# Performance work log

Measured on AMD Instinct MI355X. Metric: run time of the kernel, lower is better.

## Reference

```python
import jax, jax.numpy as jnp
import numpy as np

B, C, H, W = 8, 256, 128, 128
HEADS, WS = 8, 8
SHIFT = WS // 2  # type=='W' -> shift_size = window_size//2 in this repo
N = WS * WS


def _rel_pos_index(ws):
    coords = np.stack(np.meshgrid(np.arange(ws), np.arange(ws), indexing='ij')).reshape(2, -1)
    rel = (coords[:, :, None] - coords[:, None, :]).transpose(1, 2, 0)  # N,N,2
    rel[:, :, 0] += ws - 1
    rel[:, :, 1] += ws - 1
    rel[:, :, 0] *= 2 * ws - 1
    return rel.sum(-1)  # (N,N) ints in [0,(2ws-1)^2)


def _attn_mask(h, w, ws, shift):
    img = np.zeros((h, w), np.int32)
    cnt = 0
    for hs in (slice(0, -ws), slice(-ws, -shift), slice(-shift, None)):
        for wsl in (slice(0, -ws), slice(-ws, -shift), slice(-shift, None)):
            img[hs, wsl] = cnt
            cnt += 1
    m = img.reshape(h // ws, ws, w // ws, ws).transpose(0, 2, 1, 3).reshape(-1, ws * ws)
    diff = m[:, None, :] - m[:, :, None]
    return np.where(diff != 0, -100.0, 0.0).astype(np.float32)  # (nW,N,N)


def _ln(x, w, b, eps=1e-5):
    mu = jnp.mean(x, -1, keepdims=True)
    var = jnp.mean(jnp.square(x - mu), -1, keepdims=True)
    return (x - mu) * jax.lax.rsqrt(var + eps) * w + b


def setup_inputs() -> dict:
    key = jax.random.key(0)
    ks = jax.random.split(key, 10)
    s = 0.02
    return {
        'x': jax.random.normal(ks[0], (B, C, H, W), jnp.float32),
        'ln1_w': jnp.ones((C,), jnp.float32),
        'ln1_b': jnp.zeros((C,), jnp.float32),
        'qkv_w': jax.random.normal(ks[1], (3 * C, C), jnp.float32) * s,
        'qkv_b': jnp.zeros((3 * C,), jnp.float32),
        'rel_bias': jax.random.normal(ks[2], ((2 * WS - 1) ** 2, HEADS), jnp.float32) * s,
        'proj_w': jax.random.normal(ks[3], (C, C), jnp.float32) * s,
        'proj_b': jnp.zeros((C,), jnp.float32),
        'ln2_w': jnp.ones((C,), jnp.float32),
        'ln2_b': jnp.zeros((C,), jnp.float32),
        'fc1_w': jax.random.normal(ks[4], (4 * C, C), jnp.float32) * s,
        'fc1_b': jnp.zeros((4 * C,), jnp.float32),
        'fc2_w': jax.random.normal(ks[5], (C, 4 * C), jnp.float32) * s,
        'fc2_b': jnp.zeros((C,), jnp.float32),
    }


def reference(x, ln1_w, ln1_b, qkv_w, qkv_b, rel_bias, proj_w, proj_b,
              ln2_w, ln2_b, fc1_w, fc1_b, fc2_w, fc2_b):
    b, c, h, w = x.shape
    hd = c // HEADS
    scale = hd ** -0.5
    nW = (h // WS) * (w // WS)

    t = x.transpose(0, 2, 3, 1).reshape(b, h * w, c)  # b (hw) c
    shortcut = t
    t = _ln(t, ln1_w, ln1_b).reshape(b, h, w, c)
    t = jnp.roll(t, (-SHIFT, -SHIFT), axis=(1, 2))  # cyclic shift
    # window partition -> (b*nW, N, c)
    win = t.reshape(b, h // WS, WS, w // WS, WS, c).transpose(0, 1, 3, 2, 4, 5).reshape(b * nW, N, c)

    qkv = (win @ qkv_w.T + qkv_b).reshape(b * nW, N, 3, HEADS, hd).transpose(2, 0, 3, 1, 4)
    q, k, v = qkv[0], qkv[1], qkv[2]  # (b*nW, heads, N, hd)
    attn = jnp.einsum('bhnd,bhmd->bhnm', q * scale, k)
    rpi = jnp.asarray(_rel_pos_index(WS))
    bias = rel_bias[rpi.reshape(-1)].reshape(N, N, HEADS).transpose(2, 0, 1)  # (heads,N,N)
    attn = attn + bias[None]
    mask = jnp.asarray(_attn_mask(h, w, WS, SHIFT))  # (nW,N,N)
    attn = attn.reshape(b, nW, HEADS, N, N) + mask[None, :, None]
    attn = jax.nn.softmax(attn, axis=-1).reshape(b * nW, HEADS, N, N)
    out = jnp.einsum('bhnm,bhmd->bhnd', attn, v).transpose(0, 2, 1, 3).reshape(b * nW, N, c)
    out = out @ proj_w.T + proj_b
    # window reverse + reverse shift
    out = out.reshape(b, h // WS, w // WS, WS, WS, c).transpose(0, 1, 3, 2, 4, 5).reshape(b, h, w, c)
    out = jnp.roll(out, (SHIFT, SHIFT), axis=(1, 2)).reshape(b, h * w, c)

    t = shortcut + out
    h2 = _ln(t, ln2_w, ln2_b)
    h2 = jax.nn.gelu(h2 @ fc1_w.T + fc1_b)
    t = t + (h2 @ fc2_w.T + fc2_b)
    return t.reshape(b, h, w, c).transpose(0, 3, 1, 2)
```

## Files before the change

### kernel.cpp

```cpp
#include <hip/hip_runtime.h>
#include <cstdint>
#include <cstddef>

using f32x4 = __attribute__((ext_vector_type(4))) float;
using bf16x8 = __attribute__((ext_vector_type(8))) __bf16;
using u16x4 = __attribute__((ext_vector_type(4))) unsigned short;
using u16x8 = __attribute__((ext_vector_type(8))) unsigned short;

#define DEV __device__ __forceinline__

DEV unsigned short f2b(float f) {
  __bf16 h = (__bf16)f;
  return __builtin_bit_cast(unsigned short, h);
}
DEV float b2f(unsigned short u) {
  uint32_t w = ((uint32_t)u) << 16;
  return __builtin_bit_cast(float, w);
}

DEV void gload16(const unsigned short* g, unsigned short* l) {
  __builtin_amdgcn_global_load_lds(
      (const __attribute__((address_space(1))) void*)g,
      (__attribute__((address_space(3))) void*)l, 16, 0, 0);
}

DEV void waitv(int n) {
  switch (n) {
    case 0: asm volatile("s_waitcnt vmcnt(0)" ::: "memory"); break;
    case 2: asm volatile("s_waitcnt vmcnt(2)" ::: "memory"); break;
    case 3: asm volatile("s_waitcnt vmcnt(3)" ::: "memory"); break;
    case 8: asm volatile("s_waitcnt vmcnt(8)" ::: "memory"); break;
    default: asm volatile("s_waitcnt vmcnt(0)" ::: "memory"); break;
  }
}


__global__ void swin_cvt_all(const float* __restrict__ qkvw, const float* __restrict__ projw,
                             const float* __restrict__ fc1w, const float* __restrict__ fc2w,
                             unsigned short* __restrict__ wq, unsigned short* __restrict__ wp,
                             unsigned short* __restrict__ w1, unsigned short* __restrict__ w2) {
  int i = blockIdx.x * 256 + threadIdx.x;
  if (i < 196608) wq[i] = f2b(qkvw[i]);
  else if (i < 262144) wp[i - 196608] = f2b(projw[i - 196608]);
  else if (i < 524288) w1[i - 262144] = f2b(fc1w[i - 262144]);
  else w2[i - 524288] = f2b(fc2w[i - 524288]);
}

__global__ void swin_btab(const float* __restrict__ relb, float* __restrict__ bt) {
  int id = blockIdx.x * 256 + threadIdx.x;
  int m = id & 63, n = (id >> 6) & 63, head = (id >> 12) & 7, cls = id >> 15;
  bool eh = cls & 2, ew = cls & 1;
  int nh = n >> 3, nw = n & 7, mh = m >> 3, mw = m & 7;
  int rn = (eh ? ((nh >> 2) + 1) : 0) * 3 + (ew ? ((nw >> 2) + 1) : 0);
  int rm = (eh ? ((mh >> 2) + 1) : 0) * 3 + (ew ? ((mw >> 2) + 1) : 0);
  float v = relb[(size_t)((nh - mh + 7) * 15 + (nw - mw + 7)) * 8 + head];
  if (rn != rm) v -= 100.f;
  bt[id] = v;
}

__global__ __launch_bounds__(256)
void swin_ln1win(const float* __restrict__ x,
                 const float* __restrict__ lw, const float* __restrict__ lb,
                 unsigned short* __restrict__ win, unsigned short* __restrict__ xb) {
  __shared__ float sh[512];
  __shared__ float mean_[128], rstd_[128];
  __shared__ unsigned short tile[128 * 136];
  int bh = blockIdx.x; int b = bh >> 7, h = bh & 127;
  int t = threadIdx.x;
  int w = t & 127, ch = t >> 7;
  const float* px = x + (((size_t)(b * 256 + ch * 128)) << 14) + (h << 7) + w;
  float s = 0.f, s2 = 0.f;
  for (int c = 0; c < 128; ++c) {
    float v = px[(size_t)c << 14];
    s += v; s2 += v * v;
  }
  sh[t] = s; sh[256 + t] = s2;
  __syncthreads();
  if (ch == 0) {
    s += sh[t + 128]; s2 += sh[256 + t + 128];
    float mu = s * (1.f / 256.f);
    mean_[w] = mu;
    rstd_[w] = rsqrtf(s2 * (1.f / 256.f) - mu * mu + 1e-5f);
  }
  int hp = (h + 124) & 127;
  int whh = hp >> 3, nh = hp & 7;
  int lg = t & 31, grp = t >> 5;
#pragma unroll
  for (int half = 0; half < 2; ++half) {
    int c0 = half << 7;
    __syncthreads();
#pragma unroll
    for (int i = 0; i < 64; ++i) {
      int cr = (i << 1) + ch;
      float v = x[(((size_t)(b * 256 + c0 + cr)) << 14) + (h << 7) + w];
      tile[w * 136 + cr] = f2b(v);
    }
    __syncthreads();
#pragma unroll
    for (int i = 0; i < 16; ++i) {
      int w2 = (i << 3) + grp;
      u16x4 raw = *(const u16x4*)&tile[w2 * 136 + (lg << 2)];
      float mu = mean_[w2], rs = rstd_[w2];
      int c = c0 + (lg << 2);
      f32x4 lwv = *(const f32x4*)(lw + c);
      f32x4 lbv = *(const f32x4*)(lb + c);
      u16x4 o;
#pragma unroll
      for (int k = 0; k < 4; ++k)
        o[k] = f2b((b2f(raw[k]) - mu) * rs * lwv[k] + lbv[k]);
      int wp_ = (w2 + 124) & 127;
      int wwc = wp_ >> 3, nw = wp_ & 7;
      size_t wt = (size_t)b * 256 + whh * 16 + wwc;
      int n = (nh << 3) + nw;
      *(u16x4*)&win[((wt << 6) + n) * 256 + c] = o;
      *(u16x4*)&xb[(((size_t)bh << 7) + w2) * 256 + c] = raw;
    }
  }
}

template<int MODE, int KTOT>
__global__ __launch_bounds__(512, 2)
void swin_gemm(const unsigned short* __restrict__ A,
               const unsigned short* __restrict__ Wt,
               const float* __restrict__ bias,
               void* __restrict__ outp,
               const void* __restrict__ extra,
               int M, int N,
               const float* __restrict__ lw2 = nullptr,
               const float* __restrict__ lb2 = nullptr,
               unsigned short* __restrict__ tn = nullptr) {
  constexpr int KT = KTOT / 64;
  __shared__ __align__(16) unsigned short As[2][16384];
  __shared__ __align__(16) unsigned short Bs[2][16384];
  const int cpx = gridDim.x >> 3;
  const int bid = (blockIdx.x & 7) * cpx + (blockIdx.x >> 3);
  const int nbn = N >> 8;
  const int bm = bid / nbn;
  const int bn = bid % nbn;
  const int m0 = bm << 8, n0 = bn << 8;
  const int t = threadIdx.x;
  const int lane = t & 63;
  const int wave = t >> 6;
  const int wr = wave >> 2, wc = wave & 3;
  const int cl = lane & 15, g = lane >> 4;

  const int trow = t >> 3;
  const int ks = (t & 7) ^ (trow & 7);
  const unsigned short* agb = A  + (size_t)(m0 + trow) * KTOT + ks * 8;
  const unsigned short* bgb = Wt + (size_t)(n0 + trow) * KTOT + ks * 8;

  const int ra = wr * 128 + cl;
  const int rb = wc * 64 + cl;
  const int ka0 = (g ^ (cl & 7)) * 8;

  auto stage = [&](int buf, int kt) {
    const int ko = kt * 64;
#pragma unroll
    for (int l = 0; l < 4; ++l) {
      gload16(agb + (size_t)l * 64 * KTOT + ko, &As[buf][l * 4096 + t * 8]);
      gload16(bgb + (size_t)l * 64 * KTOT + ko, &Bs[buf][l * 4096 + t * 8]);
    }
  };

  f32x4 acc[8][4] = {};
  bf16x8 afA[8], bfA[4], afB[8], bfB[4];

  auto RD = [&](int buf, int kk, bf16x8* af, bf16x8* bfr) {
    const int ka = ka0 ^ (kk << 5);
#pragma unroll
    for (int i = 0; i < 8; ++i)
      af[i] = *(const bf16x8*)&As[buf][(ra + i * 16) * 64 + ka];
#pragma unroll
    for (int j = 0; j < 4; ++j)
      bfr[j] = *(const bf16x8*)&Bs[buf][(rb + j * 16) * 64 + ka];
  };
  auto MF = [&](bf16x8* af, bf16x8* bfr) {
    __builtin_amdgcn_s_setprio(1);
#pragma unroll
    for (int i = 0; i < 8; ++i)
#pragma unroll
      for (int j = 0; j < 4; ++j)
        acc[i][j] = __builtin_amdgcn_mfma_f32_16x16x32_bf16(bfr[j], af[i], acc[i][j], 0, 0, 0);
    __builtin_amdgcn_s_setprio(0);
  };

  stage(0, 0);
  stage(1, 1);
  waitv(8);
  __builtin_amdgcn_s_barrier();
  RD(0, 0, afA, bfA);
#pragma unroll
  for (int kt = 0; kt < KT; ++kt) {
    const int cur = kt & 1;
    RD(cur, 1, afB, bfB);
    MF(afA, bfA);
    asm volatile("s_waitcnt lgkmcnt(0)" ::: "memory");
    __builtin_amdgcn_sched_barrier(0);
    __builtin_amdgcn_s_barrier();
    if (kt + 2 < KT) stage(cur, kt + 2);
    if (kt + 1 < KT) waitv(8);
    else             waitv(0);
    __builtin_amdgcn_s_barrier();
    if (kt + 1 < KT) RD(cur ^ 1, 0, afA, bfA);
    MF(afB, bfB);
  }

  if constexpr (MODE == 1) {
    float s[8], s2v[8];
#pragma unroll
    for (int i = 0; i < 8; ++i) { s[i] = 0.f; s2v[i] = 0.f; }
#pragma unroll
    for (int i = 0; i < 8; ++i) {
      int row = m0 + wr * 128 + i * 16 + cl;
#pragma unroll
      for (int j = 0; j < 4; ++j) {
        int colb = wc * 64 + j * 16 + (g << 2);
        f32x4 b4 = *(const f32x4*)(bias + colb);
        u16x4 xv = *(const u16x4*)((const unsigned short*)extra + (size_t)row * 256 + colb);
#pragma unroll
        for (int r = 0; r < 4; ++r) {
          float v = acc[i][j][r] + b4[r] + b2f(xv[r]);
          acc[i][j][r] = v;
          s[i] += v; s2v[i] += v * v;
        }
      }
    }
#pragma unroll
    for (int i = 0; i < 8; ++i) {
      s[i]  += __shfl_xor(s[i], 16);  s[i]  += __shfl_xor(s[i], 32);
      s2v[i] += __shfl_xor(s2v[i], 16); s2v[i] += __shfl_xor(s2v[i], 32);
    }
    __syncthreads();
    float* lsum = (float*)&As[0][0];
    if (g == 0) {
#pragma unroll
      for (int i = 0; i < 8; ++i) {
        int rl = wr * 128 + i * 16 + cl;
        lsum[wc * 256 + rl] = s[i];
        lsum[1024 + wc * 256 + rl] = s2v[i];
      }
    }
    __syncthreads();
#pragma unroll
    for (int i = 0; i < 8; ++i) {
      int rl = wr * 128 + i * 16 + cl;
      float ts = lsum[rl] + lsum[256 + rl] + lsum[512 + rl] + lsum[768 + rl];
      float ts2 = lsum[1024 + rl] + lsum[1280 + rl] + lsum[1536 + rl] + lsum[1792 + rl];
      float mu = ts * (1.f / 256.f);
      float rstd = rsqrtf(ts2 * (1.f / 256.f) - mu * mu + 1e-5f);
      int row = m0 + rl;
#pragma unroll
      for (int j = 0; j < 4; ++j) {
        int colb = wc * 64 + j * 16 + (g << 2);
        f32x4 wv = *(const f32x4*)(lw2 + colb);
        f32x4 bv = *(const f32x4*)(lb2 + colb);
        u16x4 oT, on;
#pragma unroll
        for (int r = 0; r < 4; ++r) {
          float v = acc[i][j][r];
          oT[r] = f2b(v);
          on[r] = f2b((v - mu) * rstd * wv[r] + bv[r]);
        }
        *(u16x4*)((unsigned short*)outp + (size_t)row * 256 + colb) = oT;
        *(u16x4*)(tn + (size_t)row * 256 + colb) = on;
      }
    }
  } else {
#pragma unroll
    for (int i = 0; i < 8; ++i) {
      int row = m0 + wr * 128 + i * 16 + cl;
#pragma unroll
      for (int j = 0; j < 4; ++j) {
        int colb = n0 + wc * 64 + j * 16 + (g << 2);
        f32x4 b4 = *(const f32x4*)(bias + colb);
        const bool qs = (n0 == 0);
        u16x4 o;
#pragma unroll
        for (int r = 0; r < 4; ++r) {
          float v = acc[i][j][r] + b4[r];
          if (qs) v *= 0.17677669529663687f;
          o[r] = f2b(v);
        }
        *(u16x4*)((unsigned short*)outp + (size_t)row * 768 + colb) = o;
      }
    }
  }
}

__global__ __launch_bounds__(512, 2)
void swin_ffn(const unsigned short* __restrict__ tn,
              const unsigned short* __restrict__ w1,
              const unsigned short* __restrict__ w2,
              const float* __restrict__ b1,
              const float* __restrict__ b2,
              const unsigned short* __restrict__ T,
              float* __restrict__ out) {
  __shared__ __align__(16) unsigned short As[2][4096];
  __shared__ __align__(16) unsigned short Bs[2][8192];
  __shared__ __align__(16) unsigned short Hs[32768];
  const int cpx = gridDim.x >> 3;
  const int bid = (blockIdx.x & 7) * cpx + (blockIdx.x >> 3);
  const int m0 = bid << 7;
  const int t = threadIdx.x;
  const int lane = t & 63;
  const int wave = t >> 6;
  const int wr = wave >> 2, wc = wave & 3;
  const int cl = lane & 15, g = lane >> 4;

  const int arow = t >> 2;
  const int ks = (t & 3) ^ ((arow >> 1) & 3);
  const unsigned short* ag = tn + (size_t)(m0 + arow) * 256 + ks * 8;

  const int ka = (g ^ ((cl >> 1) & 3)) * 8;
  const int ra = wr * 64 + cl;
  const int rb = wc * 64 + cl;

  auto stage1 = [&](int buf, int q, int kt) {
    gload16(ag + kt * 32, &As[buf][t * 8]);
    const unsigned short* wg = w1 + (size_t)(q * 256 + arow) * 256 + kt * 32 + ks * 8;
    gload16(wg, &Bs[buf][t * 8]);
    gload16(wg + 32768, &Bs[buf][4096 + t * 8]);
  };
  auto stage2 = [&](int buf, int q, int kt) {
    const unsigned short* wg = w2 + (size_t)arow * 1024 + q * 256 + kt * 32 + ks * 8;
    gload16(wg, &Bs[buf][t * 8]);
    gload16(wg + 131072, &Bs[buf][4096 + t * 8]);
  };

  f32x4 acc2[4][4] = {};
  bf16x8 af[4], bf[4];

  auto RD1 = [&](int buf) {
#pragma unroll
    for (int i = 0; i < 4; ++i)
      af[i] = *(const bf16x8*)&As[buf][(ra + i * 16) * 32 + ka];
#pragma unroll
    for (int j = 0; j < 4; ++j)
      bf[j] = *(const bf16x8*)&Bs[buf][(rb + j * 16) * 32 + ka];
  };
  auto RD2 = [&](int buf, int kt) {
#pragma unroll
    for (int i = 0; i < 4; ++i) {
      int row = ra + i * 16;
      int c = (kt * 4 + g) ^ (row & 7);
      af[i] = *(const bf16x8*)((const char*)Hs + row * 512 + c * 16);
    }
#pragma unroll
    for (int j = 0; j < 4; ++j)
      bf[j] = *(const bf16x8*)&Bs[buf][(rb + j * 16) * 32 + ka];
  };

  for (int q = 0; q < 4; ++q) {
    f32x4 acc1[4][4] = {};
    stage1(0, q, 0); stage1(1, q, 1);
#pragma unroll
    for (int kt = 0; kt < 8; ++kt) {
      const int cur = kt & 1;
      waitv(kt < 7 ? 3 : 0);
      __builtin_amdgcn_s_barrier();
      RD1(cur);
      asm volatile("s_waitcnt lgkmcnt(0)" ::: "memory");
      __builtin_amdgcn_sched_barrier(0);
      __builtin_amdgcn_s_barrier();
      if (kt + 2 < 8) stage1(cur, q, kt + 2);
      __builtin_amdgcn_s_setprio(1);
#pragma unroll
      for (int i = 0; i < 4; ++i)
#pragma unroll
        for (int j = 0; j < 4; ++j)
          acc1[i][j] = __builtin_amdgcn_mfma_f32_16x16x32_bf16(bf[j], af[i], acc1[i][j], 0, 0, 0);
      __builtin_amdgcn_s_setprio(0);
    }
    stage2(0, q, 0); stage2(1, q, 1);
#pragma unroll
    for (int i = 0; i < 4; ++i) {
      int row = wr * 64 + i * 16 + cl;
#pragma unroll
      for (int j = 0; j < 4; ++j) {
        int colb = wc * 64 + j * 16 + (g << 2);
        f32x4 b4 = *(const f32x4*)(b1 + q * 256 + colb);
        u16x4 o;
#pragma unroll
        for (int r = 0; r < 4; ++r) {
          float v = acc1[i][j][r] + b4[r];
          float p = v * fmaf(v * v, -0.0713548256f, -1.5957691216f);
          float e = __expf(p);
          o[r] = f2b(v * __builtin_amdgcn_rcpf(1.f + e));
        }
        int swz = (colb >> 3) ^ (row & 7);
        *(u16x4*)((char*)Hs + row * 512 + swz * 16 + ((g & 1) * 8)) = o;
      }
    }
    asm volatile("s_waitcnt lgkmcnt(0)" ::: "memory");
    __builtin_amdgcn_sched_barrier(0);
    __builtin_amdgcn_s_barrier();
#pragma unroll
    for (int kt = 0; kt < 8; ++kt) {
      const int cur = kt & 1;
      waitv(kt < 7 ? 2 : 0);
      __builtin_amdgcn_s_barrier();
      RD2(cur, kt);
      asm volatile("s_waitcnt lgkmcnt(0)" ::: "memory");
      __builtin_amdgcn_sched_barrier(0);
      __builtin_amdgcn_s_barrier();
      if (kt + 2 < 8) stage2(cur, q, kt + 2);
      __builtin_amdgcn_s_setprio(1);
#pragma unroll
      for (int i = 0; i < 4; ++i)
#pragma unroll
        for (int j = 0; j < 4; ++j)
          acc2[i][j] = __builtin_amdgcn_mfma_f32_16x16x32_bf16(bf[j], af[i], acc2[i][j], 0, 0, 0);
      __builtin_amdgcn_s_setprio(0);
    }
  }

#pragma unroll
  for (int i = 0; i < 4; ++i) {
    int row = m0 + wr * 64 + i * 16 + cl;
    int b = row >> 14, hw = row & 16383;
#pragma unroll
    for (int j = 0; j < 4; ++j) {
      int colb = wc * 64 + j * 16 + (g << 2);
      f32x4 b4 = *(const f32x4*)(b2 + colb);
      u16x4 tv = *(const u16x4*)(T + (size_t)row * 256 + colb);
#pragma unroll
      for (int r = 0; r < 4; ++r)
        out[((size_t)(b * 256 + colb + r) << 14) + hw] = acc2[i][j][r] + b4[r] + b2f(tv[r]);
    }
  }
}

__global__ __launch_bounds__(256)
void swin_attn(const unsigned short* __restrict__ qkv,
               const float* __restrict__ btab,
               unsigned short* __restrict__ attn_out) {
  __shared__ unsigned short Plds[4][64 * 68];
  __shared__ unsigned short Vlds[4][32 * 68];
  int bid = blockIdx.x;
  int w = bid >> 1, hg = bid & 1;
  int t = threadIdx.x;
  int wave = t >> 6, lane = t & 63;
  int head = (hg << 2) + wave;
  int cl = lane & 15, g = lane >> 4;
  const size_t wb = (size_t)w * 64 * 768;

  bf16x8 qf[4], kf[4];
#pragma unroll
  for (int ni = 0; ni < 4; ++ni) {
    int n = (ni << 4) + cl;
    qf[ni] = *(const bf16x8*)(qkv + wb + (size_t)n * 768 + (head << 5) + (g << 3));
    kf[ni] = *(const bf16x8*)(qkv + wb + (size_t)n * 768 + 256 + (head << 5) + (g << 3));
  }

  f32x4 s[4][4] = {};
#pragma unroll
  for (int mi = 0; mi < 4; ++mi)
#pragma unroll
    for (int ni = 0; ni < 4; ++ni)
      s[mi][ni] = __builtin_amdgcn_mfma_f32_16x16x32_bf16(kf[mi], qf[ni], s[mi][ni], 0, 0, 0);

#pragma unroll
  for (int c = 0; c < 4; ++c) {
    int id = (c << 6) + lane;
    int m = id >> 2, dc = (id & 3) << 3;
    u16x8 vv = *(const u16x8*)(qkv + wb + (size_t)m * 768 + 512 + (head << 5) + dc);
#pragma unroll
    for (int j = 0; j < 8; ++j)
      Vlds[wave][(dc + j) * 68 + m] = vv[j];
  }

  int wi = w & 255;
  int cls = (((wi >> 4) == 15) ? 2 : 0) + (((wi & 15) == 15) ? 1 : 0);
  const float* bt = btab + (((size_t)(cls << 3) + head) << 12);
#pragma unroll
  for (int ni = 0; ni < 4; ++ni) {
    int n = (ni << 4) + cl;
    float mx = -1e30f;
#pragma unroll
    for (int mi = 0; mi < 4; ++mi) {
      f32x4 bb = *(const f32x4*)&bt[n * 64 + (mi << 4) + (g << 2)];
#pragma unroll
      for (int r = 0; r < 4; ++r) {
        float v = s[mi][ni][r] + bb[r];
        s[mi][ni][r] = v;
        mx = fmaxf(mx, v);
      }
    }
    mx = fmaxf(mx, __shfl_xor(mx, 16));
    mx = fmaxf(mx, __shfl_xor(mx, 32));
    float sum = 0.f;
#pragma unroll
    for (int mi = 0; mi < 4; ++mi)
#pragma unroll
      for (int r = 0; r < 4; ++r) {
        float p = __expf(s[mi][ni][r] - mx);
        s[mi][ni][r] = p;
        sum += p;
      }
    sum += __shfl_xor(sum, 16);
    sum += __shfl_xor(sum, 32);
    float inv = __builtin_amdgcn_rcpf(sum);
#pragma unroll
    for (int mi = 0; mi < 4; ++mi) {
      u16x4 pk;
#pragma unroll
      for (int r = 0; r < 4; ++r) pk[r] = f2b(s[mi][ni][r] * inv);
      *(u16x4*)&Plds[wave][n * 68 + (mi << 4) + (g << 2)] = pk;
    }
  }
  __syncthreads();

  union FragU { bf16x8 v; uint64_t q[2]; };
  f32x4 o[4][2] = {};
#pragma unroll
  for (int mt = 0; mt < 2; ++mt) {
    FragU vf[2];
#pragma unroll
    for (int dt = 0; dt < 2; ++dt) {
      int d = (dt << 4) + cl;
      const unsigned short* p = &Vlds[wave][d * 68 + (mt << 5) + (g << 3)];
      vf[dt].q[0] = *(const uint64_t*)p;
      vf[dt].q[1] = *(const uint64_t*)(p + 4);
    }
#pragma unroll
    for (int ni = 0; ni < 4; ++ni) {
      FragU pa;
      const unsigned short* pp = &Plds[wave][((ni << 4) + cl) * 68 + (mt << 5) + (g << 3)];
      pa.q[0] = *(const uint64_t*)pp;
      pa.q[1] = *(const uint64_t*)(pp + 4);
#pragma unroll
      for (int dt = 0; dt < 2; ++dt)
        o[ni][dt] = __builtin_amdgcn_mfma_f32_16x16x32_bf16(pa.v, vf[dt].v, o[ni][dt], 0, 0, 0);
    }
  }

  int b = w >> 8;
#pragma unroll
  for (int ni = 0; ni < 4; ++ni)
#pragma unroll
    for (int dt = 0; dt < 2; ++dt)
#pragma unroll
      for (int r = 0; r < 4; ++r) {
        int n = (ni << 4) + (g << 2) + r;
        int d = (dt << 4) + cl;
        int hs = ((wi >> 4) << 3) + (n >> 3), ws_ = ((wi & 15) << 3) + (n & 7);
        int hh = (hs + 4) & 127, ww = (ws_ + 4) & 127;
        size_t tok = ((size_t)b << 14) + (hh << 7) + ww;
        attn_out[tok * 256 + (head << 5) + d] = f2b(o[ni][dt][r]);
      }
}

extern "C" void kernel_launch(void* const* d_in, const int* in_sizes, int n_in,
                              void* d_out, int out_size, void* d_ws, size_t ws_size,
                              hipStream_t stream) {
  const float* x    = (const float*)d_in[0];
  const float* ln1w = (const float*)d_in[1];
  const float* ln1b = (const float*)d_in[2];
  const float* qkvw = (const float*)d_in[3];
  const float* qkvb = (const float*)d_in[4];
  const float* relb = (const float*)d_in[5];
  const float* projw = (const float*)d_in[6];
  const float* projb = (const float*)d_in[7];
  const float* ln2w = (const float*)d_in[8];
  const float* ln2b = (const float*)d_in[9];
  const float* fc1w = (const float*)d_in[10];
  const float* fc1b = (const float*)d_in[11];
  const float* fc2w = (const float*)d_in[12];
  const float* fc2b = (const float*)d_in[13];

  char* ws = (char*)d_ws;
  unsigned short* win = (unsigned short*)(ws);
  unsigned short* qkv = (unsigned short*)(ws + 67108864);
  unsigned short* T   = (unsigned short*)(ws + 268435456);
  unsigned short* xb  = (unsigned short*)(ws + 335544320);
  unsigned short* wq  = (unsigned short*)(ws + 402653184);
  unsigned short* wp  = (unsigned short*)(ws + 403046400);
  unsigned short* w1  = (unsigned short*)(ws + 403177472);
  unsigned short* w2  = (unsigned short*)(ws + 403701760);
  float* btab         = (float*)(ws + 404226048);
  unsigned short* attn_out = win;
  unsigned short* tn  = (unsigned short*)(ws + 67108864);

  if (ws_size < 404750336ull) return;

  swin_cvt_all<<<3072, 256, 0, stream>>>(qkvw, projw, fc1w, fc2w, wq, wp, w1, w2);
  swin_btab<<<512, 256, 0, stream>>>(relb, btab);
  swin_ln1win<<<1024, 256, 0, stream>>>(x, ln1w, ln1b, win, xb);
  swin_gemm<0, 256><<<1536, 512, 0, stream>>>(win, wq, qkvb, qkv, nullptr, 131072, 768);
  swin_attn<<<4096, 256, 0, stream>>>(qkv, btab, attn_out);
  swin_gemm<1, 256><<<512, 512, 0, stream>>>(attn_out, wp, projb, T, xb, 131072, 256,
                                             ln2w, ln2b, tn);
  swin_ffn<<<1024, 512, 0, stream>>>(tn, w1, w2, fc1b, fc2b, T, (float*)d_out);
}
```

Measured before the change: 578.0 us.

## Fuse QKV projection into windowed attention kernel and retile FFN second GEMM

Replaces the separate QKV GEMM and attention kernels with a single per-window kernel. Each block loads one 64-token window into LDS, computes Q/K/V for all 8 heads with MFMA reading weights straight from global, and runs softmax attention from LDS, so the large QKV intermediate never round-trips through HBM. The proj GEMM is specialised to N=256. The FFN second GEMM now uses 64-wide K tiles with a per-quarter hidden layout, larger B staging and fewer pipeline steps. The trade-offs are that the fused kernel uses about 130KB of LDS per block, which limits occupancy, and it re-reads the QKV weights from global/L2 for every window.

New measurement: 539.8 us. -6.6%, faster.

```diff
diff --git a/kernel.cpp b/kernel.cpp
--- a/kernel.cpp
+++ b/kernel.cpp
@@ -27,8 +27,8 @@
 DEV void waitv(int n) {
   switch (n) {
     case 0: asm volatile("s_waitcnt vmcnt(0)" ::: "memory"); break;
-    case 2: asm volatile("s_waitcnt vmcnt(2)" ::: "memory"); break;
     case 3: asm volatile("s_waitcnt vmcnt(3)" ::: "memory"); break;
+    case 4: asm volatile("s_waitcnt vmcnt(4)" ::: "memory"); break;
     case 8: asm volatile("s_waitcnt vmcnt(8)" ::: "memory"); break;
     default: asm volatile("s_waitcnt vmcnt(0)" ::: "memory"); break;
   }
@@ -118,26 +118,195 @@
   }
 }
 
-template<int MODE, int KTOT>
+__global__ __launch_bounds__(512)
+void swin_qkvattn(const unsigned short* __restrict__ win,
+                  const unsigned short* __restrict__ wq,
+                  const float* __restrict__ qkvb,
+                  const float* __restrict__ btab,
+                  unsigned short* __restrict__ attn_out) {
+  __shared__ __align__(16) char L[133120];
+  const int wt = blockIdx.x;
+  const int t = threadIdx.x;
+  const int lane = t & 63;
+  const int head = t >> 6;
+  const int cl = lane & 15, g = lane >> 4;
+
+  {
+    const unsigned short* src = win + (size_t)wt * 16384;
+    int row = t >> 3;
+    int sch = (t & 7) ^ (row & 7);
+#pragma unroll
+    for (int o = 0; o < 4; ++o)
+      gload16(src + row * 256 + o * 64 + sch * 8,
+              (unsigned short*)(L + o * 8192 + t * 16));
+  }
+  __syncthreads();
+
+  f32x4 acc1[4][6] = {};
+#pragma unroll
+  for (int kt = 0; kt < 8; ++kt) {
+    bf16x8 af[4], bf[6];
+    const char* sub = L + (kt >> 1) * 8192;
+    const int kc = (kt & 1) * 4 + g;
+#pragma unroll
+    for (int i = 0; i < 4; ++i) {
+      int tok = i * 16 + cl;
+      af[i] = *(const bf16x8*)(sub + tok * 128 + ((kc ^ (tok & 7)) * 16));
+    }
+#pragma unroll
+    for (int j = 0; j < 6; ++j) {
+      int col = (j >> 1) * 256 + head * 32 + (j & 1) * 16 + cl;
+      bf[j] = *(const bf16x8*)(wq + (size_t)col * 256 + kt * 32 + g * 8);
+    }
+#pragma unroll
+    for (int i = 0; i < 4; ++i)
+#pragma unroll
+      for (int j = 0; j < 6; ++j)
+        acc1[i][j] = __builtin_amdgcn_mfma_f32_16x16x32_bf16(bf[j], af[i], acc1[i][j], 0, 0, 0);
+  }
+
+  char* hb = L + 32768 + head * 12544;
+#pragma unroll
+  for (int i = 0; i < 4; ++i) {
+    int tok = i * 16 + cl;
+#pragma unroll
+    for (int j = 0; j < 6; ++j) {
+      int p = j >> 1;
+      int c32b = (j & 1) * 16 + (g << 2);
+      f32x4 b4 = *(const f32x4*)(qkvb + p * 256 + head * 32 + c32b);
+      if (p < 2) {
+        u16x4 o;
+#pragma unroll
+        for (int r = 0; r < 4; ++r) {
+          float v = acc1[i][j][r] + b4[r];
+          if (p == 0) v *= 0.17677669529663687f;
+          o[r] = f2b(v);
+        }
+        int chunk = ((j & 1) * 2 + (g >> 1)) ^ ((tok >> 1) & 3);
+        *(u16x4*)(hb + p * 4096 + tok * 64 + chunk * 16 + (g & 1) * 8) = o;
+      } else {
+        unsigned short* vt = (unsigned short*)(hb + 8192);
+#pragma unroll
+        for (int r = 0; r < 4; ++r)
+          vt[(c32b + r) * 68 + tok] = f2b(acc1[i][j][r] + b4[r]);
+      }
+    }
+  }
+  asm volatile("s_waitcnt lgkmcnt(0)" ::: "memory");
+  __builtin_amdgcn_sched_barrier(0);
+
+  bf16x8 qf[4], kf[4];
+#pragma unroll
+  for (int ni = 0; ni < 4; ++ni) {
+    int tok = (ni << 4) + cl;
+    int chunk = g ^ ((tok >> 1) & 3);
+    qf[ni] = *(const bf16x8*)(hb + tok * 64 + chunk * 16);
+    kf[ni] = *(const bf16x8*)(hb + 4096 + tok * 64 + chunk * 16);
+  }
+  f32x4 s[4][4] = {};
+#pragma unroll
+  for (int mi = 0; mi < 4; ++mi)
+#pragma unroll
+    for (int ni = 0; ni < 4; ++ni)
+      s[mi][ni] = __builtin_amdgcn_mfma_f32_16x16x32_bf16(kf[mi], qf[ni], s[mi][ni], 0, 0, 0);
+
+  int wi = wt & 255;
+  int cls = (((wi >> 4) == 15) ? 2 : 0) + (((wi & 15) == 15) ? 1 : 0);
+  const float* bt = btab + (((size_t)(cls << 3) + head) << 12);
+#pragma unroll
+  for (int ni = 0; ni < 4; ++ni) {
+    int n = (ni << 4) + cl;
+    float mx = -1e30f;
+#pragma unroll
+    for (int mi = 0; mi < 4; ++mi) {
+      f32x4 bb = *(const f32x4*)&bt[n * 64 + (mi << 4) + (g << 2)];
+#pragma unroll
+      for (int r = 0; r < 4; ++r) {
+        float v = s[mi][ni][r] + bb[r];
+        s[mi][ni][r] = v;
+        mx = fmaxf(mx, v);
+      }
+    }
+    mx = fmaxf(mx, __shfl_xor(mx, 16));
+    mx = fmaxf(mx, __shfl_xor(mx, 32));
+    float sum = 0.f;
+#pragma unroll
+    for (int mi = 0; mi < 4; ++mi)
+#pragma unroll
+      for (int r = 0; r < 4; ++r) {
+        float p = __expf(s[mi][ni][r] - mx);
+        s[mi][ni][r] = p;
+        sum += p;
+      }
+    sum += __shfl_xor(sum, 16);
+    sum += __shfl_xor(sum, 32);
+    float inv = __builtin_amdgcn_rcpf(sum);
+#pragma unroll
+    for (int mi = 0; mi < 4; ++mi) {
+      u16x4 pk;
+#pragma unroll
+      for (int r = 0; r < 4; ++r) pk[r] = f2b(s[mi][ni][r] * inv);
+      int chunk = (mi * 2 + (g >> 1)) ^ (n & 7);
+      *(u16x4*)(hb + n * 128 + chunk * 16 + (g & 1) * 8) = pk;
+    }
+  }
+  asm volatile("s_waitcnt lgkmcnt(0)" ::: "memory");
+  __builtin_amdgcn_sched_barrier(0);
+
+  union FragU { bf16x8 v; uint64_t q[2]; };
+  f32x4 o[4][2] = {};
+  const unsigned short* vt = (const unsigned short*)(hb + 8192);
+#pragma unroll
+  for (int mt = 0; mt < 2; ++mt) {
+    FragU vf[2];
+#pragma unroll
+    for (int dt = 0; dt < 2; ++dt) {
+      int d = (dt << 4) + cl;
+      const unsigned short* p = vt + d * 68 + (mt << 5) + (g << 3);
+      vf[dt].q[0] = *(const uint64_t*)p;
+      vf[dt].q[1] = *(const uint64_t*)(p + 4);
+    }
+#pragma unroll
+    for (int ni = 0; ni < 4; ++ni) {
+      int n = (ni << 4) + cl;
+      int chunk = (mt * 4 + g) ^ (n & 7);
+      bf16x8 pa = *(const bf16x8*)(hb + n * 128 + chunk * 16);
+#pragma unroll
+      for (int dt = 0; dt < 2; ++dt)
+        o[ni][dt] = __builtin_amdgcn_mfma_f32_16x16x32_bf16(pa, vf[dt].v, o[ni][dt], 0, 0, 0);
+    }
+  }
+
+  int b = wt >> 8;
+#pragma unroll
+  for (int ni = 0; ni < 4; ++ni)
+#pragma unroll
+    for (int dt = 0; dt < 2; ++dt)
+#pragma unroll
+      for (int r = 0; r < 4; ++r) {
+        int n = (ni << 4) + (g << 2) + r;
+        int d = (dt << 4) + cl;
+        int hs = ((wi >> 4) << 3) + (n >> 3), ws_ = ((wi & 15) << 3) + (n & 7);
+        int hh = (hs + 4) & 127, ww = (ws_ + 4) & 127;
+        size_t tok = ((size_t)b << 14) + (hh << 7) + ww;
+        attn_out[tok * 256 + (head << 5) + d] = f2b(o[ni][dt][r]);
+      }
+}
+
 __global__ __launch_bounds__(512, 2)
-void swin_gemm(const unsigned short* __restrict__ A,
+void swin_proj(const unsigned short* __restrict__ A,
                const unsigned short* __restrict__ Wt,
                const float* __restrict__ bias,
-               void* __restrict__ outp,
-               const void* __restrict__ extra,
-               int M, int N,
-               const float* __restrict__ lw2 = nullptr,
-               const float* __restrict__ lb2 = nullptr,
-               unsigned short* __restrict__ tn = nullptr) {
-  constexpr int KT = KTOT / 64;
+               unsigned short* __restrict__ T,
+               const unsigned short* __restrict__ xb,
+               const float* __restrict__ lw2, const float* __restrict__ lb2,
+               unsigned short* __restrict__ tn) {
+  constexpr int KT = 4;
   __shared__ __align__(16) unsigned short As[2][16384];
   __shared__ __align__(16) unsigned short Bs[2][16384];
   const int cpx = gridDim.x >> 3;
   const int bid = (blockIdx.x & 7) * cpx + (blockIdx.x >> 3);
-  const int nbn = N >> 8;
-  const int bm = bid / nbn;
-  const int bn = bid % nbn;
-  const int m0 = bm << 8, n0 = bn << 8;
+  const int m0 = bid << 8;
   const int t = threadIdx.x;
   const int lane = t & 63;
   const int wave = t >> 6;
@@ -146,8 +315,8 @@
 
   const int trow = t >> 3;
   const int ks = (t & 7) ^ (trow & 7);
-  const unsigned short* agb = A  + (size_t)(m0 + trow) * KTOT + ks * 8;
-  const unsigned short* bgb = Wt + (size_t)(n0 + trow) * KTOT + ks * 8;
+  const unsigned short* agb = A  + (size_t)(m0 + trow) * 256 + ks * 8;
+  const unsigned short* bgb = Wt + (size_t)trow * 256 + ks * 8;
 
   const int ra = wr * 128 + cl;
   const int rb = wc * 64 + cl;
@@ -157,8 +326,8 @@
     const int ko = kt * 64;
 #pragma unroll
     for (int l = 0; l < 4; ++l) {
-      gload16(agb + (size_t)l * 64 * KTOT + ko, &As[buf][l * 4096 + t * 8]);
-      gload16(bgb + (size_t)l * 64 * KTOT + ko, &Bs[buf][l * 4096 + t * 8]);
+      gload16(agb + (size_t)l * 64 * 256 + ko, &As[buf][l * 4096 + t * 8]);
+      gload16(bgb + (size_t)l * 64 * 256 + ko, &Bs[buf][l * 4096 + t * 8]);
     }
   };
 
@@ -205,89 +374,68 @@
     MF(afB, bfB);
   }
 
-  if constexpr (MODE == 1) {
-    float s[8], s2v[8];
-#pragma unroll
-    for (int i = 0; i < 8; ++i) { s[i] = 0.f; s2v[i] = 0.f; }
-#pragma unroll
-    for (int i = 0; i < 8; ++i) {
-      int row = m0 + wr * 128 + i * 16 + cl;
-#pragma unroll
-      for (int j = 0; j < 4; ++j) {
-        int colb = wc * 64 + j * 16 + (g << 2);
-        f32x4 b4 = *(const f32x4*)(bias + colb);
-        u16x4 xv = *(const u16x4*)((const unsigned short*)extra + (size_t)row * 256 + colb);
-#pragma unroll
-        for (int r = 0; r < 4; ++r) {
-          float v = acc[i][j][r] + b4[r] + b2f(xv[r]);
-          acc[i][j][r] = v;
-          s[i] += v; s2v[i] += v * v;
-        }
-      }
-    }
-#pragma unroll
-    for (int i = 0; i < 8; ++i) {
-      s[i]  += __shfl_xor(s[i], 16);  s[i]  += __shfl_xor(s[i], 32);
-      s2v[i] += __shfl_xor(s2v[i], 16); s2v[i] += __shfl_xor(s2v[i], 32);
-    }
-    __syncthreads();
-    float* lsum = (float*)&As[0][0];
-    if (g == 0) {
-#pragma unroll
-      for (int i = 0; i < 8; ++i) {
-        int rl = wr * 128 + i * 16 + cl;
-        lsum[wc * 256 + rl] = s[i];
-        lsum[1024 + wc * 256 + rl] = s2v[i];
-      }
-    }
-    __syncthreads();
+  float s[8], s2v[8];
+#pragma unroll
+  for (int i = 0; i < 8; ++i) { s[i] = 0.f; s2v[i] = 0.f; }
+#pragma unroll
+  for (int i = 0; i < 8; ++i) {
+    int row = m0 + wr * 128 + i * 16 + cl;
+#pragma unroll
+    for (int j = 0; j < 4; ++j) {
+      int colb = wc * 64 + j * 16 + (g << 2);
+      f32x4 b4 = *(const f32x4*)(bias + colb);
+      u16x4 xv = *(const u16x4*)(xb + (size_t)row * 256 + colb);
+#pragma unroll
+      for (int r = 0; r < 4; ++r) {
+        float v = acc[i][j][r] + b4[r] + b2f(xv[r]);
+        acc[i][j][r] = v;
+        s[i] += v; s2v[i] += v * v;
+      }
+    }
+  }
+#pragma unroll
+  for (int i = 0; i < 8; ++i) {
+    s[i]  += __shfl_xor(s[i], 16);  s[i]  += __shfl_xor(s[i], 32);
+    s2v[i] += __shfl_xor(s2v[i], 16); s2v[i] += __shfl_xor(s2v[i], 32);
+  }
+  __syncthreads();
+  float* lsum = (float*)&As[0][0];
+  if (g == 0) {
 #pragma unroll
     for (int i = 0; i < 8; ++i) {
       int rl = wr * 128 + i * 16 + cl;
-      float ts = lsum[rl] + lsum[256 + rl] + lsum[512 + rl] + lsum[768 + rl];
-      float ts2 = lsum[1024 + rl] + lsum[1280 + rl] + lsum[1536 + rl] + lsum[1792 + rl];
-      float mu = ts * (1.f / 256.f);
-      float rstd = rsqrtf(ts2 * (1.f / 256.f) - mu * mu + 1e-5f);
-      int row = m0 + rl;
-#pragma unroll
-      for (int j = 0; j < 4; ++j) {
-        int colb = wc * 64 + j * 16 + (g << 2);
-        f32x4 wv = *(const f32x4*)(lw2 + colb);
-        f32x4 bv = *(const f32x4*)(lb2 + colb);
-        u16x4 oT, on;
-#pragma unroll
-        for (int r = 0; r < 4; ++r) {
-          float v = acc[i][j][r];
-          oT[r] = f2b(v);
-          on[r] = f2b((v - mu) * rstd * wv[r] + bv[r]);
-        }
-        *(u16x4*)((unsigned short*)outp + (size_t)row * 256 + colb) = oT;
-        *(u16x4*)(tn + (size_t)row * 256 + colb) = on;
-      }
-    }
-  } else {
-#pragma unroll
-    for (int i = 0; i < 8; ++i) {
-      int row = m0 + wr * 128 + i * 16 + cl;
-#pragma unroll
-      for (int j = 0; j < 4; ++j) {
-        int colb = n0 + wc * 64 + j * 16 + (g << 2);
-        f32x4 b4 = *(const f32x4*)(bias + colb);
-        const bool qs = (n0 == 0);
-        u16x4 o;
-#pragma unroll
-        for (int r = 0; r < 4; ++r) {
-          float v = acc[i][j][r] + b4[r];
-          if (qs) v *= 0.17677669529663687f;
-          o[r] = f2b(v);
-        }
-        *(u16x4*)((unsigned short*)outp + (size_t)row * 768 + colb) = o;
-      }
-    }
-  }
-}
-
-__global__ __launch_bounds__(512, 2)
+      lsum[wc * 256 + rl] = s[i];
+      lsum[1024 + wc * 256 + rl] = s2v[i];
+    }
+  }
+  __syncthreads();
+#pragma unroll
+  for (int i = 0; i < 8; ++i) {
+    int rl = wr * 128 + i * 16 + cl;
+    float ts = lsum[rl] + lsum[256 + rl] + lsum[512 + rl] + lsum[768 + rl];
+    float ts2 = lsum[1024 + rl] + lsum[1280 + rl] + lsum[1536 + rl] + lsum[1792 + rl];
+    float mu = ts * (1.f / 256.f);
+    float rstd = rsqrtf(ts2 * (1.f / 256.f) - mu * mu + 1e-5f);
+    int row = m0 + rl;
+#pragma unroll
+    for (int j = 0; j < 4; ++j) {
+      int colb = wc * 64 + j * 16 + (g << 2);
+      f32x4 wv = *(const f32x4*)(lw2 + colb);
+      f32x4 bv = *(const f32x4*)(lb2 + colb);
+      u16x4 oT, on;
+#pragma unroll
+      for (int r = 0; r < 4; ++r) {
+        float v = acc[i][j][r];
+        oT[r] = f2b(v);
+        on[r] = f2b((v - mu) * rstd * wv[r] + bv[r]);
+      }
+      *(u16x4*)(T + (size_t)row * 256 + colb) = oT;
+      *(u16x4*)(tn + (size_t)row * 256 + colb) = on;
+    }
+  }
+}
+
+__global__ __launch_bounds__(512)
 void swin_ffn(const unsigned short* __restrict__ tn,
               const unsigned short* __restrict__ w1,
               const unsigned short* __restrict__ w2,
@@ -296,7 +444,7 @@
               const unsigned short* __restrict__ T,
               float* __restrict__ out) {
   __shared__ __align__(16) unsigned short As[2][4096];
-  __shared__ __align__(16) unsigned short Bs[2][8192];
+  __shared__ __align__(16) unsigned short Bs[2][16384];
   __shared__ __align__(16) unsigned short Hs[32768];
   const int cpx = gridDim.x >> 3;
   const int bid = (blockIdx.x & 7) * cpx + (blockIdx.x >> 3);
@@ -314,6 +462,8 @@
   const int ka = (g ^ ((cl >> 1) & 3)) * 8;
   const int ra = wr * 64 + cl;
   const int rb = wc * 64 + cl;
+  const int brow = t >> 3;
+  const int bch = (t & 7) ^ (brow & 7);
 
   auto stage1 = [&](int buf, int q, int kt) {
     gload16(ag + kt * 32, &As[buf][t * 8]);
@@ -322,33 +472,14 @@
     gload16(wg + 32768, &Bs[buf][4096 + t * 8]);
   };
   auto stage2 = [&](int buf, int q, int kt) {
-    const unsigned short* wg = w2 + (size_t)arow * 1024 + q * 256 + kt * 32 + ks * 8;
-    gload16(wg, &Bs[buf][t * 8]);
-    gload16(wg + 131072, &Bs[buf][4096 + t * 8]);
+#pragma unroll
+    for (int l = 0; l < 4; ++l) {
+      const unsigned short* wg = w2 + (size_t)(l * 64 + brow) * 1024 + q * 256 + kt * 64 + bch * 8;
+      gload16(wg, &Bs[buf][l * 4096 + t * 8]);
+    }
   };
 
   f32x4 acc2[4][4] = {};
-  bf16x8 af[4], bf[4];
-
-  auto RD1 = [&](int buf) {
-#pragma unroll
-    for (int i = 0; i < 4; ++i)
-      af[i] = *(const bf16x8*)&As[buf][(ra + i * 16) * 32 + ka];
-#pragma unroll
-    for (int j = 0; j < 4; ++j)
-      bf[j] = *(const bf16x8*)&Bs[buf][(rb + j * 16) * 32 + ka];
-  };
-  auto RD2 = [&](int buf, int kt) {
-#pragma unroll
-    for (int i = 0; i < 4; ++i) {
-      int row = ra + i * 16;
-      int c = (kt * 4 + g) ^ (row & 7);
-      af[i] = *(const bf16x8*)((const char*)Hs + row * 512 + c * 16);
-    }
-#pragma unroll
-    for (int j = 0; j < 4; ++j)
-      bf[j] = *(const bf16x8*)&Bs[buf][(rb + j * 16) * 32 + ka];
-  };
 
   for (int q = 0; q < 4; ++q) {
     f32x4 acc1[4][4] = {};
@@ -358,7 +489,13 @@
       const int cur = kt & 1;
       waitv(kt < 7 ? 3 : 0);
       __builtin_amdgcn_s_barrier();
-      RD1(cur);
+      bf16x8 af[4], bf[4];
+#pragma unroll
+      for (int i = 0; i < 4; ++i)
+        af[i] = *(const bf16x8*)&As[cur][(ra + i * 16) * 32 + ka];
+#pragma unroll
+      for (int j = 0; j < 4; ++j)
+        bf[j] = *(const bf16x8*)&Bs[cur][(rb + j * 16) * 32 + ka];
       asm volatile("s_waitcnt lgkmcnt(0)" ::: "memory");
       __builtin_amdgcn_sched_barrier(0);
       __builtin_amdgcn_s_barrier();
@@ -377,8 +514,7 @@
       int row = wr * 64 + i * 16 + cl;
 #pragma unroll
       for (int j = 0; j < 4; ++j) {
-        int colb = wc * 64 + j * 16 + (g << 2);
-        f32x4 b4 = *(const f32x4*)(b1 + q * 256 + colb);
+        f32x4 b4 = *(const f32x4*)(b1 + q * 256 + wc * 64 + j * 16 + (g << 2));
         u16x4 o;
 #pragma unroll
         for (int r = 0; r < 4; ++r) {
@@ -387,29 +523,47 @@
           float e = __expf(p);
           o[r] = f2b(v * __builtin_amdgcn_rcpf(1.f + e));
         }
-        int swz = (colb >> 3) ^ (row & 7);
-        *(u16x4*)((char*)Hs + row * 512 + swz * 16 + ((g & 1) * 8)) = o;
+        int chunk = (j * 2 + (g >> 1)) ^ (row & 7);
+        *(u16x4*)((char*)Hs + wc * 16384 + row * 128 + chunk * 16 + (g & 1) * 8) = o;
       }
     }
     asm volatile("s_waitcnt lgkmcnt(0)" ::: "memory");
     __builtin_amdgcn_sched_barrier(0);
     __builtin_amdgcn_s_barrier();
 #pragma unroll
-    for (int kt = 0; kt < 8; ++kt) {
+    for (int kt = 0; kt < 4; ++kt) {
       const int cur = kt & 1;
-      waitv(kt < 7 ? 2 : 0);
+      waitv(kt < 3 ? 4 : 0);
       __builtin_amdgcn_s_barrier();
-      RD2(cur, kt);
+      bf16x8 af2[4][2], bf2[4][2];
+#pragma unroll
+      for (int i = 0; i < 4; ++i) {
+        int row = ra + i * 16;
+#pragma unroll
+        for (int kk = 0; kk < 2; ++kk)
+          af2[i][kk] = *(const bf16x8*)((const char*)Hs + kt * 16384 + row * 128 +
+                                        (((kk * 4 + g) ^ (row & 7)) * 16));
+      }
+#pragma unroll
+      for (int j = 0; j < 4; ++j) {
+        int row = rb + j * 16;
+#pragma unroll
+        for (int kk = 0; kk < 2; ++kk)
+          bf2[j][kk] = *(const bf16x8*)&Bs[cur][row * 64 + (((kk * 4 + g) ^ (cl & 7)) * 8)];
+      }
       asm volatile("s_waitcnt lgkmcnt(0)" ::: "memory");
       __builtin_amdgcn_sched_barrier(0);
       __builtin_amdgcn_s_barrier();
-      if (kt + 2 < 8) stage2(cur, q, kt + 2);
+      if (kt + 2 < 4) stage2(cur, q, kt + 2);
       __builtin_amdgcn_s_setprio(1);
 #pragma unroll
-      for (int i = 0; i < 4; ++i)
-#pragma unroll
-        for (int j = 0; j < 4; ++j)
-          acc2[i][j] = __builtin_amdgcn_mfma_f32_16x16x32_bf16(bf[j], af[i], acc2[i][j], 0, 0, 0);
+      for (int kk = 0; kk < 2; ++kk)
+#pragma unroll
+        for (int i = 0; i < 4; ++i)
+#pragma unroll
+          for (int j = 0; j < 4; ++j)
+            acc2[i][j] = __builtin_amdgcn_mfma_f32_16x16x32_bf16(bf2[j][kk], af2[i][kk],
+                                                                 acc2[i][j], 0, 0, 0);
       __builtin_amdgcn_s_setprio(0);
     }
   }
@@ -428,126 +582,6 @@
         out[((size_t)(b * 256 + colb + r) << 14) + hw] = acc2[i][j][r] + b4[r] + b2f(tv[r]);
     }
   }
-}
-
-__global__ __launch_bounds__(256)
-void swin_attn(const unsigned short* __restrict__ qkv,
-               const float* __restrict__ btab,
-               unsigned short* __restrict__ attn_out) {
-  __shared__ unsigned short Plds[4][64 * 68];
-  __shared__ unsigned short Vlds[4][32 * 68];
-  int bid = blockIdx.x;
-  int w = bid >> 1, hg = bid & 1;
-  int t = threadIdx.x;
-  int wave = t >> 6, lane = t & 63;
-  int head = (hg << 2) + wave;
-  int cl = lane & 15, g = lane >> 4;
-  const size_t wb = (size_t)w * 64 * 768;
-
-  bf16x8 qf[4], kf[4];
-#pragma unroll
-  for (int ni = 0; ni < 4; ++ni) {
-    int n = (ni << 4) + cl;
-    qf[ni] = *(const bf16x8*)(qkv + wb + (size_t)n * 768 + (head << 5) + (g << 3));
-    kf[ni] = *(const bf16x8*)(qkv + wb + (size_t)n * 768 + 256 + (head << 5) + (g << 3));
-  }
-
-  f32x4 s[4][4] = {};
-#pragma unroll
-  for (int mi = 0; mi < 4; ++mi)
-#pragma unroll
-    for (int ni = 0; ni < 4; ++ni)
-      s[mi][ni] = __builtin_amdgcn_mfma_f32_16x16x32_bf16(kf[mi], qf[ni], s[mi][ni], 0, 0, 0);
-
-#pragma unroll
-  for (int c = 0; c < 4; ++c) {
-    int id = (c << 6) + lane;
-    int m = id >> 2, dc = (id & 3) << 3;
-    u16x8 vv = *(const u16x8*)(qkv + wb + (size_t)m * 768 + 512 + (head << 5) + dc);
-#pragma unroll
-    for (int j = 0; j < 8; ++j)
-      Vlds[wave][(dc + j) * 68 + m] = vv[j];
-  }
-
-  int wi = w & 255;
-  int cls = (((wi >> 4) == 15) ? 2 : 0) + (((wi & 15) == 15) ? 1 : 0);
-  const float* bt = btab + (((size_t)(cls << 3) + head) << 12);
-#pragma unroll
-  for (int ni = 0; ni < 4; ++ni) {
-    int n = (ni << 4) + cl;
-    float mx = -1e30f;
-#pragma unroll
-    for (int mi = 0; mi < 4; ++mi) {
-      f32x4 bb = *(const f32x4*)&bt[n * 64 + (mi << 4) + (g << 2)];
-#pragma unroll
-      for (int r = 0; r < 4; ++r) {
-        float v = s[mi][ni][r] + bb[r];
-        s[mi][ni][r] = v;
-        mx = fmaxf(mx, v);
-      }
-    }
-    mx = fmaxf(mx, __shfl_xor(mx, 16));
-    mx = fmaxf(mx, __shfl_xor(mx, 32));
-    float sum = 0.f;
-#pragma unroll
-    for (int mi = 0; mi < 4; ++mi)
-#pragma unroll
-      for (int r = 0; r < 4; ++r) {
-        float p = __expf(s[mi][ni][r] - mx);
-        s[mi][ni][r] = p;
-        sum += p;
-      }
-    sum += __shfl_xor(sum, 16);
-    sum += __shfl_xor(sum, 32);
-    float inv = __builtin_amdgcn_rcpf(sum);
-#pragma unroll
-    for (int mi = 0; mi < 4; ++mi) {
-      u16x4 pk;
-#pragma unroll
-      for (int r = 0; r < 4; ++r) pk[r] = f2b(s[mi][ni][r] * inv);
-      *(u16x4*)&Plds[wave][n * 68 + (mi << 4) + (g << 2)] = pk;
-    }
-  }
-  __syncthreads();
-
-  union FragU { bf16x8 v; uint64_t q[2]; };
-  f32x4 o[4][2] = {};
-#pragma unroll
-  for (int mt = 0; mt < 2; ++mt) {
-    FragU vf[2];
-#pragma unroll
-    for (int dt = 0; dt < 2; ++dt) {
-      int d = (dt << 4) + cl;
-      const unsigned short* p = &Vlds[wave][d * 68 + (mt << 5) + (g << 3)];
-      vf[dt].q[0] = *(const uint64_t*)p;
-      vf[dt].q[1] = *(const uint64_t*)(p + 4);
-    }
-#pragma unroll
-    for (int ni = 0; ni < 4; ++ni) {
-      FragU pa;
-      const unsigned short* pp = &Plds[wave][((ni << 4) + cl) * 68 + (mt << 5) + (g << 3)];
-      pa.q[0] = *(const uint64_t*)pp;
-      pa.q[1] = *(const uint64_t*)(pp + 4);
-#pragma unroll
-      for (int dt = 0; dt < 2; ++dt)
-        o[ni][dt] = __builtin_amdgcn_mfma_f32_16x16x32_bf16(pa.v, vf[dt].v, o[ni][dt], 0, 0, 0);
-    }
-  }
-
-  int b = w >> 8;
-#pragma unroll
-  for (int ni = 0; ni < 4; ++ni)
-#pragma unroll
-    for (int dt = 0; dt < 2; ++dt)
-#pragma unroll
-      for (int r = 0; r < 4; ++r) {
-        int n = (ni << 4) + (g << 2) + r;
-        int d = (dt << 4) + cl;
-        int hs = ((wi >> 4) << 3) + (n >> 3), ws_ = ((wi & 15) << 3) + (n & 7);
-        int hh = (hs + 4) & 127, ww = (ws_ + 4) & 127;
-        size_t tok = ((size_t)b << 14) + (hh << 7) + ww;
-        attn_out[tok * 256 + (head << 5) + d] = f2b(o[ni][dt][r]);
-      }
 }
 
 extern "C" void kernel_launch(void* const* d_in, const int* in_sizes, int n_in,
@@ -569,26 +603,23 @@
   const float* fc2b = (const float*)d_in[13];
 
   char* ws = (char*)d_ws;
-  unsigned short* win = (unsigned short*)(ws);
-  unsigned short* qkv = (unsigned short*)(ws + 67108864);
-  unsigned short* T   = (unsigned short*)(ws + 268435456);
-  unsigned short* xb  = (unsigned short*)(ws + 335544320);
+  unsigned short* win      = (unsigned short*)(ws);
+  unsigned short* attn_out = (unsigned short*)(ws + 67108864);
+  unsigned short* tn       = (unsigned short*)(ws + 134217728);
+  unsigned short* T        = (unsigned short*)(ws + 268435456);
+  unsigned short* xb       = (unsigned short*)(ws + 335544320);
   unsigned short* wq  = (unsigned short*)(ws + 402653184);
   unsigned short* wp  = (unsigned short*)(ws + 403046400);
   unsigned short* w1  = (unsigned short*)(ws + 403177472);
   unsigned short* w2  = (unsigned short*)(ws + 403701760);
   float* btab         = (float*)(ws + 404226048);
-  unsigned short* attn_out = win;
-  unsigned short* tn  = (unsigned short*)(ws + 67108864);
 
   if (ws_size < 404750336ull) return;
 
   swin_cvt_all<<<3072, 256, 0, stream>>>(qkvw, projw, fc1w, fc2w, wq, wp, w1, w2);
   swin_btab<<<512, 256, 0, stream>>>(relb, btab);
   swin_ln1win<<<1024, 256, 0, stream>>>(x, ln1w, ln1b, win, xb);
-  swin_gemm<0, 256><<<1536, 512, 0, stream>>>(win, wq, qkvb, qkv, nullptr, 131072, 768);
-  swin_attn<<<4096, 256, 0, stream>>>(qkv, btab, attn_out);
-  swin_gemm<1, 256><<<512, 512, 0, stream>>>(attn_out, wp, projb, T, xb, 131072, 256,
-                                             ln2w, ln2b, tn);
+  swin_qkvattn<<<2048, 512, 0, stream>>>(win, wq, qkvb, btab, attn_out);
+  swin_proj<<<512, 512, 0, stream>>>(attn_out, wp, projb, T, xb, ln2w, ln2b, tn);
   swin_ffn<<<1024, 512, 0, stream>>>(tn, w1, w2, fc1b, fc2b, T, (float*)d_out);
 }
```
